# Kernel optimization log

Measured on AMD Instinct MI355X. Metric: run time of the kernel, lower is better.

The kernel has to match this reference:

```python
import jax, jax.numpy as jnp
import numpy as np

CHEB_K = 2  # chebyshev polynomial order (support_ks = [I, A] for cheb_k=2)


def _fc(x, w1, b1, w2, b2, w3, b3):
    # FC module: Linear -> sigmoid -> Linear -> sigmoid -> Linear
    h = jax.nn.sigmoid(x @ w1 + b1)
    h = jax.nn.sigmoid(h @ w2 + b2)
    return h @ w3 + b3


def _preprocess(adj):
    # adj: [B,N,N]; add self-loops then row-normalize
    adj = adj + jnp.eye(adj.shape[-1], dtype=adj.dtype)
    return adj / adj.sum(-1, keepdims=True)


def _gcn(x, adjs, ne, wpool, bpool):
    # x: [B,N,C], adjs: list of [B,N,N], ne: [N,E]
    # wpool: [E, 2*CHEB_K, C, O], bpool: [E, O]
    mats = []
    for A in adjs:
        ks = [jnp.broadcast_to(jnp.eye(A.shape[-1], dtype=A.dtype), A.shape), A]
        for _ in range(2, CHEB_K):
            ks.append(2.0 * jnp.matmul(A, ks[-1]) - ks[-2])
        mats.extend(ks)
    # [B,N,K,C] with K = 2*CHEB_K
    x_g = jnp.stack([jnp.einsum('bnm,bmc->bnc', S, x) for S in mats], axis=2)
    weights = jnp.einsum('nd,dkio->nkio', ne, wpool)  # [N,K,C,O]
    bias = ne @ bpool  # [N,O]
    return jnp.einsum('bnki,nkio->bno', x_g, weights) + bias


def _forward(x, state, ne0, ne1, ne2, fc1_w1, fc1_b1, fc1_w2, fc1_b2, fc1_w3, fc1_b3,
             fc2_w1, fc2_b1, fc2_w2, fc2_b2, fc2_w3, fc2_b3, gate_w, gate_b, upd_w, upd_b):
    hid = upd_w.shape[-1]
    ins = jnp.concatenate([x, state], axis=-1)  # [B,N,dim_in+hid]
    f1 = _fc(ins, fc1_w1, fc1_b1, fc1_w2, fc1_b2, fc1_w3, fc1_b3)  # [B,N,TD]
    f2 = _fc(ins, fc2_w1, fc2_b1, fc2_w2, fc2_b2, fc2_w3, fc2_b3)
    nv1 = jnp.tanh(ne0[:, None, :] * f1)  # einsum 'bd,bnd->bnd' == broadcast mul
    nv2 = jnp.tanh(ne1[:, None, :] * f2)
    adj = jnp.einsum('bnd,bmd->bnm', nv1, nv2) - jnp.einsum('bnd,bmd->bnm', nv2, nv1)
    adj1 = _preprocess(jax.nn.relu(adj))
    adj2 = _preprocess(jax.nn.relu(-jnp.swapaxes(adj, -2, -1)))
    z_r = jax.nn.sigmoid(_gcn(ins, [adj1, adj2], ne2, gate_w, gate_b))
    z, r = z_r[..., :hid], z_r[..., hid:]
    cand = jnp.concatenate([x, z * state], axis=-1)
    hc = jnp.tanh(_gcn(cand, [adj1, adj2], ne2, upd_w, upd_b))
    return r * state + (1.0 - r) * hc


def setup_inputs():
    B, N, DIN, DOUT, ED, TD = 32, 1024, 2, 64, 10, 32
    HG, MID = 16, 2  # hyperGNN_dim, middle_dim hardcoded in FC
    CIN = DIN + DOUT
    K2 = 2 * CHEB_K
    ks = jax.random.split(jax.random.key(0), 16)
    rn = lambda i, shape, s=1.0: jax.random.normal(ks[i], shape, dtype=jnp.float32) * s
    return {
        'x': rn(0, (B, N, DIN)),
        'state': rn(1, (B, N, DOUT)),
        'ne0': rn(2, (B, TD)),
        'ne1': rn(3, (B, TD)),
        'ne2': rn(4, (N, ED), 0.1),
        'fc1_w1': rn(5, (CIN, HG), 0.1), 'fc1_b1': jnp.zeros((HG,), jnp.float32),
        'fc1_w2': rn(6, (HG, MID), 0.1), 'fc1_b2': jnp.zeros((MID,), jnp.float32),
        'fc1_w3': rn(7, (MID, TD), 0.1), 'fc1_b3': jnp.zeros((TD,), jnp.float32),
        'fc2_w1': rn(8, (CIN, HG), 0.1), 'fc2_b1': jnp.zeros((HG,), jnp.float32),
        'fc2_w2': rn(9, (HG, MID), 0.1), 'fc2_b2': jnp.zeros((MID,), jnp.float32),
        'fc2_w3': rn(10, (MID, TD), 0.1), 'fc2_b3': jnp.zeros((TD,), jnp.float32),
        'gate_w': rn(11, (ED, K2, CIN, 2 * DOUT), 0.1),
        'gate_b': rn(12, (ED, 2 * DOUT), 0.1),
        'upd_w': rn(13, (ED, K2, CIN, DOUT), 0.1),
        'upd_b': rn(14, (ED, DOUT), 0.1),
    }


def reference(x, state, ne0, ne1, ne2, fc1_w1, fc1_b1, fc1_w2, fc1_b2, fc1_w3, fc1_b3,
              fc2_w1, fc2_b1, fc2_w2, fc2_b2, fc2_w3, fc2_b3, gate_w, gate_b, upd_w, upd_b):
    return _forward(x, state, ne0, ne1, ne2, fc1_w1, fc1_b1, fc1_w2, fc1_b2, fc1_w3, fc1_b3,
                    fc2_w1, fc2_b1, fc2_w2, fc2_b2, fc2_w3, fc2_b3, gate_w, gate_b, upd_w, upd_b)
```

## Files before the change

### kernel.cpp

```cpp
#include <hip/hip_runtime.h>
#include <math.h>

#define BB   32
#define NN   1024
#define DIN  2
#define DOUT 64
#define CIN  66
#define TD   32
#define ED   10
#define OG   128
#define OU   64
#define KP   160
#define XTR  80

typedef __bf16 bf16x8 __attribute__((ext_vector_type(8)));
typedef float  f32x4  __attribute__((ext_vector_type(4)));
typedef short  s16x8  __attribute__((ext_vector_type(8)));

__device__ __forceinline__ unsigned short f2b(float f) {
    __bf16 h = (__bf16)f;
    return *(unsigned short*)&h;
}

__device__ __forceinline__ unsigned int cvt_pk_bf16(float lo, float hi) {
    unsigned int r;
    asm("v_cvt_pk_bf16_f32 %0, %1, %2" : "=v"(r) : "v"(lo), "v"(hi));
    return r;
}
__device__ __forceinline__ void perm32swap(unsigned int& a, unsigned int& b) {
    asm("v_permlane32_swap_b32 %0, %1" : "+v"(a), "+v"(b));
}
__device__ __forceinline__ void perm16swap(unsigned int& a, unsigned int& b) {
    asm("v_permlane16_swap_b32 %0, %1" : "+v"(a), "+v"(b));
}

__global__ __launch_bounds__(256) void k_pre(
    const float* __restrict__ x, const float* __restrict__ state,
    const float* __restrict__ ne0, const float* __restrict__ ne1,
    const float* __restrict__ ne2,
    const float* __restrict__ w11, const float* __restrict__ b11,
    const float* __restrict__ w12, const float* __restrict__ b12,
    const float* __restrict__ w13, const float* __restrict__ b13,
    const float* __restrict__ w21, const float* __restrict__ b21,
    const float* __restrict__ w22, const float* __restrict__ b22,
    const float* __restrict__ w23, const float* __restrict__ b23,
    const float* __restrict__ gate_w, const float* __restrict__ gate_b,
    const float* __restrict__ upd_w, const float* __restrict__ upd_b,
    unsigned short* __restrict__ nv1b, unsigned short* __restrict__ nv2b,
    unsigned short* __restrict__ XT0, unsigned short* __restrict__ XT1,
    unsigned short* __restrict__ BcTg, unsigned short* __restrict__ BcTu,
    float* __restrict__ biasG, float* __restrict__ biasU)
{
    __shared__ float sw[2408];
    __shared__ unsigned short st[68*72];
    int blk = blockIdx.x;
    int t = threadIdx.x;

    if (blk < 128) {
        const int oW1 = 0, oB1 = 1056, oW2 = 1072, oB2 = 1104, oW3 = 1108, oB3 = 1172, F2 = 1204;
        for (int i = t; i < 1056; i += 256) { sw[oW1+i] = w11[i]; sw[F2+oW1+i] = w21[i]; }
        if (t < 16) { sw[oB1+t] = b11[t]; sw[F2+oB1+t] = b21[t]; }
        if (t < 32) { sw[oW2+t] = w12[t]; sw[F2+oW2+t] = w22[t]; }
        if (t < 2)  { sw[oB2+t] = b12[t]; sw[F2+oB2+t] = b22[t]; }
        if (t < 64) { sw[oW3+t] = w13[t]; sw[F2+oW3+t] = w23[t]; }
        if (t >= 64 && t < 96) { sw[oB3+t-64] = b13[t-64]; sw[F2+oB3+t-64] = b23[t-64]; }
        __syncthreads();

        int p = blk*256 + t;
        int b = p >> 10;

        float h1a[16], h1b[16];
        #pragma unroll
        for (int j = 0; j < 16; ++j) { h1a[j] = sw[oB1+j]; h1b[j] = sw[F2+oB1+j]; }
        for (int i = 0; i < CIN; ++i) {
            float v = (i < DIN) ? x[(size_t)p*DIN + i] : state[(size_t)p*DOUT + (i-DIN)];
            #pragma unroll
            for (int jq = 0; jq < 4; ++jq) {
                float4 wa = *(const float4*)&sw[oW1 + i*16 + jq*4];
                float4 wb = *(const float4*)&sw[F2 + oW1 + i*16 + jq*4];
                h1a[jq*4+0] += v*wa.x; h1a[jq*4+1] += v*wa.y;
                h1a[jq*4+2] += v*wa.z; h1a[jq*4+3] += v*wa.w;
                h1b[jq*4+0] += v*wb.x; h1b[jq*4+1] += v*wb.y;
                h1b[jq*4+2] += v*wb.z; h1b[jq*4+3] += v*wb.w;
            }
        }
        #pragma unroll
        for (int j = 0; j < 16; ++j) {
            h1a[j] = 1.f/(1.f + __expf(-h1a[j]));
            h1b[j] = 1.f/(1.f + __expf(-h1b[j]));
        }
        float h2a0 = sw[oB2+0], h2a1 = sw[oB2+1];
        float h2b0 = sw[F2+oB2+0], h2b1 = sw[F2+oB2+1];
        #pragma unroll
        for (int i = 0; i < 16; ++i) {
            h2a0 += h1a[i]*sw[oW2 + i*2 + 0];
            h2a1 += h1a[i]*sw[oW2 + i*2 + 1];
            h2b0 += h1b[i]*sw[F2+oW2 + i*2 + 0];
            h2b1 += h1b[i]*sw[F2+oW2 + i*2 + 1];
        }
        h2a0 = 1.f/(1.f + __expf(-h2a0)); h2a1 = 1.f/(1.f + __expf(-h2a1));
        h2b0 = 1.f/(1.f + __expf(-h2b0)); h2b1 = 1.f/(1.f + __expf(-h2b1));

        const float* pn0 = ne0 + b*TD;
        const float* pn1 = ne1 + b*TD;
        #pragma unroll
        for (int jq = 0; jq < 8; ++jq) {
            float4 ba  = *(const float4*)&sw[oB3 + jq*4];
            float4 wa0 = *(const float4*)&sw[oW3 + jq*4];
            float4 wa1 = *(const float4*)&sw[oW3 + 32 + jq*4];
            float4 bb2 = *(const float4*)&sw[F2+oB3 + jq*4];
            float4 wb0 = *(const float4*)&sw[F2+oW3 + jq*4];
            float4 wb1 = *(const float4*)&sw[F2+oW3 + 32 + jq*4];
            float4 n0 = *(const float4*)&pn0[jq*4];
            float4 n1 = *(const float4*)&pn1[jq*4];
            ushort4 u1, u2;
            u1.x = f2b(tanhf(n0.x*(ba.x + h2a0*wa0.x + h2a1*wa1.x)));
            u1.y = f2b(tanhf(n0.y*(ba.y + h2a0*wa0.y + h2a1*wa1.y)));
            u1.z = f2b(tanhf(n0.z*(ba.z + h2a0*wa0.z + h2a1*wa1.z)));
            u1.w = f2b(tanhf(n0.w*(ba.w + h2a0*wa0.w + h2a1*wa1.w)));
            u2.x = f2b(tanhf(n1.x*(bb2.x + h2b0*wb0.x + h2b1*wb1.x)));
            u2.y = f2b(tanhf(n1.y*(bb2.y + h2b0*wb0.y + h2b1*wb1.y)));
            u2.z = f2b(tanhf(n1.z*(bb2.z + h2b0*wb0.z + h2b1*wb1.z)));
            u2.w = f2b(tanhf(n1.w*(bb2.w + h2b0*wb0.w + h2b1*wb1.w)));
            *(ushort4*)&nv1b[(size_t)p*TD + jq*4] = u1;
            *(ushort4*)&nv2b[(size_t)p*TD + jq*4] = u2;
        }
    } else if (blk < 640) {
        int idx = blk - 128;
        int b = idx >> 4, m0 = (idx & 15)*64;
        for (int i = t; i < 1024; i += 256) {
            int m = i >> 4, cq = i & 15;
            size_t base = (size_t)b*NN + m0 + m;
            float4 v = *(const float4*)&state[base*DOUT + cq*4];
            st[(2 + cq*4 + 0)*72 + m] = f2b(v.x);
            st[(2 + cq*4 + 1)*72 + m] = f2b(v.y);
            st[(2 + cq*4 + 2)*72 + m] = f2b(v.z);
            st[(2 + cq*4 + 3)*72 + m] = f2b(v.w);
        }
        if (t < 128) {
            int m = t >> 1, c = t & 1;
            st[c*72 + m] = f2b(x[((size_t)b*NN + m0 + m)*DIN + c]);
        }
        __syncthreads();
        const unsigned int ONE2 = 0x3F803F80u;
        for (int i = t; i < XTR*8; i += 256) {
            int c = i >> 3, ch = i & 7;
            uint4 v;
            if (c < 66)      v = *(const uint4*)&st[c*72 + ch*8];
            else if (c == 66) v = make_uint4(ONE2, ONE2, ONE2, ONE2);
            else              v = make_uint4(0, 0, 0, 0);
            *(uint4*)&XT0[((size_t)b*XTR + c)*NN + m0 + ch*8] = v;
            if (c < 2 || c >= 66)
                *(uint4*)&XT1[((size_t)b*XTR + c)*NN + m0 + ch*8] = v;
        }
    } else if (blk < 1840) {
        int tid = (blk - 640)*256 + t;
        int c = tid / KP, k = tid - c*KP;
        const float* pool; int O, cc; unsigned short* dst;
        if (c < 1280) { pool = gate_w; O = OG; cc = c;        dst = BcTg; }
        else          { pool = upd_w;  O = OU; cc = c - 1280; dst = BcTu; }
        int d = cc / O, o = cc - d*O;
        float v = 0.f;
        if (k < 132) {
            int kp = (k < 66) ? 0 : 1;
            int i  = (k < 66) ? k : k - 66;
            v = pool[(size_t)((d*4 + kp)*CIN + i)*O + o]
              + pool[(size_t)((d*4 + kp + 2)*CIN + i)*O + o];
        }
        dst[(size_t)cc*KP + k] = f2b(v);
    } else {
        int i = (blk - 1840)*256 + t;
        int n = i / 192, j = i - n*192;
        float v = 0.f;
        if (j < 128) {
            #pragma unroll
            for (int d = 0; d < ED; ++d) v += ne2[(size_t)n*ED + d]*gate_b[d*OG + j];
            biasG[(size_t)n*OG + j] = v;
        } else {
            int o = j - 128;
            #pragma unroll
            for (int d = 0; d < ED; ++d) v += ne2[(size_t)n*ED + d]*upd_b[d*OU + o];
            biasU[(size_t)n*OU + o] = v;
        }
    }
}

__global__ __launch_bounds__(256) void k_aapply(
    const unsigned short* __restrict__ nv1b, const unsigned short* __restrict__ nv2b,
    const unsigned short* __restrict__ XTg, unsigned short* __restrict__ A)
{
    __shared__ unsigned short s_nv1c[2][2560];
    __shared__ unsigned short s_nv2c[2][2560];
    __shared__ unsigned short s_xt[2][5760];

    int t = threadIdx.x;
    int id = blockIdx.x;
    int b = id & 31, rbase = (id >> 5)*64;
    int w = t >> 6, lane = t & 63, lq = lane >> 4, ln = lane & 15;

    bf16x8 a1 = *(const bf16x8*)&nv1b[((size_t)b*NN + rbase + 16*w + ln)*TD + lq*8];
    s16x8 a2s = *(const s16x8*)&nv2b[((size_t)b*NN + rbase + 16*w + ln)*TD + lq*8];
    const s16x8 sgn = {(short)0x8000,(short)0x8000,(short)0x8000,(short)0x8000,
                       (short)0x8000,(short)0x8000,(short)0x8000,(short)0x8000};
    a2s ^= sgn;
    bf16x8 a2n = (bf16x8)a2s;

    const unsigned short* pnv1 = nv1b + (size_t)b*NN*TD;
    const unsigned short* pnv2 = nv2b + (size_t)b*NN*TD;
    const unsigned short* pxt  = XTg  + (size_t)b*XTR*NN;
    int nnode = t >> 2;
    int nch   = (t & 3)*8;
    int xc    = t >> 3;
    int xch   = (t & 7)*8;

    uint4 q0, q1, r0, r1, r2;

    f32x4 acc[5];
    #pragma unroll
    for (int k = 0; k < 5; ++k) acc[k] = (f32x4){0.f,0.f,0.f,0.f};
    const f32x4 zero4 = {0.f,0.f,0.f,0.f};
    union U8 { unsigned int u[4]; bf16x8 v; };

    q0 = *(const uint4*)&pnv1[(size_t)nnode*TD + nch];
    q1 = *(const uint4*)&pnv2[(size_t)nnode*TD + nch];
    r0 = *(const uint4*)&pxt[(size_t)xc*NN + xch];
    r1 = *(const uint4*)&pxt[(size_t)(xc+32)*NN + xch];
    if (t < 128) r2 = *(const uint4*)&pxt[(size_t)(xc+64)*NN + xch];
    *(uint4*)&s_nv1c[0][nnode*40 + nch] = q0;
    *(uint4*)&s_nv2c[0][nnode*40 + nch] = q1;
    *(uint4*)&s_xt[0][xc*72 + xch] = r0;
    *(uint4*)&s_xt[0][(xc+32)*72 + xch] = r1;
    if (t < 128) *(uint4*)&s_xt[0][(xc+64)*72 + xch] = r2;
    q0 = *(const uint4*)&pnv1[(size_t)(64 + nnode)*TD + nch];
    q1 = *(const uint4*)&pnv2[(size_t)(64 + nnode)*TD + nch];
    r0 = *(const uint4*)&pxt[(size_t)xc*NN + 64 + xch];
    r1 = *(const uint4*)&pxt[(size_t)(xc+32)*NN + 64 + xch];
    if (t < 128) r2 = *(const uint4*)&pxt[(size_t)(xc+64)*NN + 64 + xch];
    __syncthreads();

    int cur = 0;
    for (int mb = 0; mb < NN; mb += 64) {
        if (mb + 64 < NN) {
            *(uint4*)&s_nv1c[cur^1][nnode*40 + nch] = q0;
            *(uint4*)&s_nv2c[cur^1][nnode*40 + nch] = q1;
            *(uint4*)&s_xt[cur^1][xc*72 + xch] = r0;
            *(uint4*)&s_xt[cur^1][(xc+32)*72 + xch] = r1;
            if (t < 128) *(uint4*)&s_xt[cur^1][(xc+64)*72 + xch] = r2;
        }
        if (mb + 128 < NN) {
            int mb2 = mb + 128;
            q0 = *(const uint4*)&pnv1[(size_t)(mb2 + nnode)*TD + nch];
            q1 = *(const uint4*)&pnv2[(size_t)(mb2 + nnode)*TD + nch];
            r0 = *(const uint4*)&pxt[(size_t)xc*NN + mb2 + xch];
            r1 = *(const uint4*)&pxt[(size_t)(xc+32)*NN + mb2 + xch];
            if (t < 128) r2 = *(const uint4*)&pxt[(size_t)(xc+64)*NN + mb2 + xch];
        }

        unsigned int u[4][2];
        #pragma unroll
        for (int jj = 0; jj < 4; ++jj) {
            bf16x8 b2 = *(const bf16x8*)&s_nv2c[cur][(jj*16 + ln)*40 + lq*8];
            bf16x8 b1 = *(const bf16x8*)&s_nv1c[cur][(jj*16 + ln)*40 + lq*8];
            f32x4 s = __builtin_amdgcn_mfma_f32_16x16x32_bf16(b2, a1,  zero4, 0, 0, 0);
            s       = __builtin_amdgcn_mfma_f32_16x16x32_bf16(b1, a2n, s,     0, 0, 0);
            u[jj][0] = cvt_pk_bf16(fmaxf(s[0], 0.f), fmaxf(s[1], 0.f));
            u[jj][1] = cvt_pk_bf16(fmaxf(s[2], 0.f), fmaxf(s[3], 0.f));
        }

        unsigned int w00 = u[0][0], w20 = u[1][0]; perm32swap(w00, w20); perm16swap(w00, w20);
        unsigned int w01 = u[0][1], w21 = u[1][1]; perm32swap(w01, w21); perm16swap(w01, w21);
        unsigned int x00 = u[2][0], x20 = u[3][0]; perm32swap(x00, x20); perm16swap(x00, x20);
        unsigned int x01 = u[2][1], x21 = u[3][1]; perm32swap(x01, x21); perm16swap(x01, x21);
        U8 p0, p1;
        p0.u[0] = w00; p0.u[1] = w01; p0.u[2] = w20; p0.u[3] = w21;
        p1.u[0] = x00; p1.u[1] = x01; p1.u[2] = x20; p1.u[3] = x21;
        bf16x8 pa0 = p0.v, pa1 = p1.v;

        #pragma unroll
        for (int k = 0; k < 5; ++k) {
            bf16x8 xb0 = *(const bf16x8*)&s_xt[cur][(k*16 + ln)*72 +      lq*8];
            bf16x8 xb1 = *(const bf16x8*)&s_xt[cur][(k*16 + ln)*72 + 32 + lq*8];
            acc[k] = __builtin_amdgcn_mfma_f32_16x16x32_bf16(pa0, xb0, acc[k], 0, 0, 0);
            acc[k] = __builtin_amdgcn_mfma_f32_16x16x32_bf16(pa1, xb1, acc[k], 0, 0, 0);
        }

        __syncthreads();
        cur ^= 1;
    }

    float rinv[4];
    #pragma unroll
    for (int r = 0; r < 4; ++r) {
        float rs = __shfl(acc[4][r], (lane & 48) | 2, 64);
        rinv[r] = 1.0f / (1.0f + rs);
    }

    #pragma unroll
    for (int k = 0; k < 5; ++k) {
        int c = k*16 + ln;
        if (c < CIN) {
            #pragma unroll
            for (int r = 0; r < 4; ++r) {
                int gr = rbase + 16*w + lq*4 + r;
                size_t rowG = (size_t)b*NN + gr;
                unsigned short xu = XTg[((size_t)b*XTR + c)*NN + gr];
                float xr = (float)(*(const __bf16*)&xu);
                A[rowG*KP + c]      = xu;
                A[rowG*KP + 66 + c] = f2b((acc[k][r] + xr) * rinv[r]);
            }
        }
    }
    for (int i = t; i < 64*28; i += 256) {
        int rr = i / 28, cc = 132 + (i - 28*(i/28));
        A[((size_t)b*NN + rbase + rr)*KP + cc] = 0;
    }
}

template<int O, int MODE>
__global__ __launch_bounds__(256) void k_gemm(
    const unsigned short* __restrict__ A, const unsigned short* __restrict__ BcT,
    const float* __restrict__ ne2, const float* __restrict__ biasP,
    const float* __restrict__ state, unsigned short* __restrict__ XT1,
    float* __restrict__ rbuf, float* __restrict__ out)
{
    __shared__ unsigned short s_b[80*168];

    int t = threadIdx.x;
    int w = t >> 6, lane = t & 63, lq = lane >> 4, ln = lane & 15;
    int o0 = blockIdx.y*16;
    int rowBlock = blockIdx.x*128;
    int rowW = rowBlock + w*32;

    f32x4 acc[2][2][5];
    #pragma unroll
    for (int h = 0; h < 2; ++h)
        #pragma unroll
        for (int f = 0; f < 2; ++f)
            #pragma unroll
            for (int c = 0; c < 5; ++c) acc[h][f][c] = (f32x4){0.f,0.f,0.f,0.f};

    #pragma unroll
    for (int h = 0; h < 2; ++h) {
        if (h) __syncthreads();
        for (int i = t; i < 1600; i += 256) {
            int cc = i / 20, kc = i - cc*20;
            int d = h*5 + (cc >> 4), oo = cc & 15;
            *(uint4*)&s_b[cc*168 + kc*8] =
                *(const uint4*)&BcT[(size_t)(d*O + o0 + oo)*KP + kc*8];
        }
        __syncthreads();

        #pragma unroll
        for (int kc = 0; kc < 5; ++kc) {
            bf16x8 af0 = *(const bf16x8*)&A[(size_t)(rowW      + ln)*KP + kc*32 + lq*8];
            bf16x8 af1 = *(const bf16x8*)&A[(size_t)(rowW + 16 + ln)*KP + kc*32 + lq*8];
            #pragma unroll
            for (int ct = 0; ct < 5; ++ct) {
                bf16x8 bf = *(const bf16x8*)&s_b[(ct*16 + ln)*168 + kc*32 + lq*8];
                acc[h][0][ct] = __builtin_amdgcn_mfma_f32_16x16x32_bf16(af0, bf, acc[h][0][ct], 0, 0, 0);
                acc[h][1][ct] = __builtin_amdgcn_mfma_f32_16x16x32_bf16(af1, bf, acc[h][1][ct], 0, 0, 0);
            }
        }
    }

    int o = o0 + ln;
    #pragma unroll
    for (int f = 0; f < 2; ++f) {
        #pragma unroll
        for (int r = 0; r < 4; ++r) {
            int row_l = w*32 + 16*f + lq*4 + r;
            size_t rowG = (size_t)rowBlock + row_l;
            int n = (int)(rowG & (NN - 1));
            int bb = (int)(rowG >> 10);
            const float* nep = &ne2[(size_t)n*ED];
            float val = biasP[(size_t)n*O + o];
            #pragma unroll
            for (int d = 0; d < 5; ++d) val += nep[d]     * acc[0][f][d][r];
            #pragma unroll
            for (int d = 0; d < 5; ++d) val += nep[5 + d] * acc[1][f][d][r];
            if (MODE == 0) {
                float sv = 1.f/(1.f + __expf(-val));
                if (o0 < 64) {
                    float zst = sv * state[rowG*DOUT + o];
                    XT1[((size_t)bb*XTR + 2 + o)*NN + n] = f2b(zst);
                } else {
                    rbuf[rowG*DOUT + (o - 64)] = sv;
                }
            } else {
                float hc = tanhf(val);
                float rg = rbuf[rowG*DOUT + o];
                float st = state[rowG*DOUT + o];
                out[rowG*DOUT + o] = rg*st + (1.f - rg)*hc;
            }
        }
    }
}

extern "C" void kernel_launch(void* const* d_in, const int* in_sizes, int n_in,
                              void* d_out, int out_size, void* d_ws, size_t ws_size,
                              hipStream_t stream)
{
    const float* x      = (const float*)d_in[0];
    const float* state  = (const float*)d_in[1];
    const float* ne0    = (const float*)d_in[2];
    const float* ne1    = (const float*)d_in[3];
    const float* ne2    = (const float*)d_in[4];
    const float* f1w1   = (const float*)d_in[5];
    const float* f1b1   = (const float*)d_in[6];
    const float* f1w2   = (const float*)d_in[7];
    const float* f1b2   = (const float*)d_in[8];
    const float* f1w3   = (const float*)d_in[9];
    const float* f1b3   = (const float*)d_in[10];
    const float* f2w1   = (const float*)d_in[11];
    const float* f2b1   = (const float*)d_in[12];
    const float* f2w2   = (const float*)d_in[13];
    const float* f2b2   = (const float*)d_in[14];
    const float* f2w3   = (const float*)d_in[15];
    const float* f2b3   = (const float*)d_in[16];
    const float* gate_w = (const float*)d_in[17];
    const float* gate_b = (const float*)d_in[18];
    const float* upd_w  = (const float*)d_in[19];
    const float* upd_b  = (const float*)d_in[20];

    unsigned short* nv1b = (unsigned short*)d_ws;
    unsigned short* nv2b = nv1b + (size_t)BB*NN*TD;
    unsigned short* XT0  = nv2b + (size_t)BB*NN*TD;
    unsigned short* XT1  = XT0  + (size_t)BB*XTR*NN;
    unsigned short* A    = XT1  + (size_t)BB*XTR*NN;
    unsigned short* BcTg = A    + (size_t)BB*NN*KP;
    unsigned short* BcTu = BcTg + (size_t)1280*KP;
    float* biasG = (float*)(BcTu + (size_t)640*KP);
    float* biasU = biasG + (size_t)NN*OG;
    float* rbuf  = biasU + (size_t)NN*OU;
    float* out   = (float*)d_out;

    k_pre<<<dim3(2608), 256, 0, stream>>>(x, state, ne0, ne1, ne2,
        f1w1, f1b1, f1w2, f1b2, f1w3, f1b3,
        f2w1, f2b1, f2w2, f2b2, f2w3, f2b3,
        gate_w, gate_b, upd_w, upd_b,
        nv1b, nv2b, XT0, XT1, BcTg, BcTu, biasG, biasU);

    k_aapply<<<dim3(512), 256, 0, stream>>>(nv1b, nv2b, XT0, A);

    k_gemm<OG,0><<<dim3(BB*NN/128, 8), 256, 0, stream>>>(A, BcTg, ne2, biasG,
                                                         state, XT1, rbuf, nullptr);

    k_aapply<<<dim3(512), 256, 0, stream>>>(nv1b, nv2b, XT1, A);

    k_gemm<OU,1><<<dim3(BB*NN/128, 4), 256, 0, stream>>>(A, BcTu, ne2, biasU,
                                                         state, nullptr, rbuf, out);
}
```

Measured before the change: 222.0 us.

## Stage A tile in LDS once and loop over output tiles with double-buffered B

The GEMM kernel previously launched one block per (row tile, 16-column output tile) and re-read the A rows from global memory for every output tile. Now each block loads its 128-row A tile into shared memory once and iterates over all output tiles. It prefetches the next B slice into registers while computing on the current one, with double-buffered LDS for B. This cuts redundant A traffic but shrinks the grid to 256 blocks, raises LDS use, and serializes output tiles per block, which may reduce occupancy and parallelism.

```diff
diff --git a/kernel.cpp b/kernel.cpp
--- a/kernel.cpp
+++ b/kernel.cpp
@@ -316,6 +316,50 @@
     }
 }
 
+__device__ __forceinline__ void gemm_half(
+    const unsigned short* sa, const unsigned short* sbh,
+    f32x4 (&acc)[2][5], int w, int lq, int ln)
+{
+    #pragma unroll
+    for (int kc = 0; kc < 5; ++kc) {
+        bf16x8 af0 = *(const bf16x8*)&sa[(w*32      + ln)*168 + kc*32 + lq*8];
+        bf16x8 af1 = *(const bf16x8*)&sa[(w*32 + 16 + ln)*168 + kc*32 + lq*8];
+        #pragma unroll
+        for (int ct = 0; ct < 5; ++ct) {
+            bf16x8 bf = *(const bf16x8*)&sbh[(ct*16 + ln)*168 + kc*32 + lq*8];
+            acc[0][ct] = __builtin_amdgcn_mfma_f32_16x16x32_bf16(af0, bf, acc[0][ct], 0, 0, 0);
+            acc[1][ct] = __builtin_amdgcn_mfma_f32_16x16x32_bf16(af1, bf, acc[1][ct], 0, 0, 0);
+        }
+    }
+}
+
+__device__ __forceinline__ void loadB(
+    const unsigned short* __restrict__ BcT, int O, int o0, int h, int t,
+    uint4 (&pr)[7])
+{
+    #pragma unroll
+    for (int k = 0; k < 7; ++k) {
+        int i = k*256 + t;
+        if (i < 1600) {
+            int cc = i/20, kc = i - cc*20;
+            int d = h*5 + (cc >> 4), oo = cc & 15;
+            pr[k] = *(const uint4*)&BcT[(size_t)(d*O + o0 + oo)*KP + kc*8];
+        }
+    }
+}
+
+__device__ __forceinline__ void writeB(unsigned short* sb, int t, const uint4 (&pr)[7])
+{
+    #pragma unroll
+    for (int k = 0; k < 7; ++k) {
+        int i = k*256 + t;
+        if (i < 1600) {
+            int cc = i/20, kc = i - cc*20;
+            *(uint4*)&sb[cc*168 + kc*8] = pr[k];
+        }
+    }
+}
+
 template<int O, int MODE>
 __global__ __launch_bounds__(256) void k_gemm(
     const unsigned short* __restrict__ A, const unsigned short* __restrict__ BcT,
@@ -323,76 +367,78 @@
     const float* __restrict__ state, unsigned short* __restrict__ XT1,
     float* __restrict__ rbuf, float* __restrict__ out)
 {
-    __shared__ unsigned short s_b[80*168];
-
+    __shared__ unsigned short s_a[128*168];
+    __shared__ unsigned short s_b[2][80*168];
+
+    const int NT = O/16;
     int t = threadIdx.x;
     int w = t >> 6, lane = t & 63, lq = lane >> 4, ln = lane & 15;
-    int o0 = blockIdx.y*16;
     int rowBlock = blockIdx.x*128;
-    int rowW = rowBlock + w*32;
-
-    f32x4 acc[2][2][5];
-    #pragma unroll
-    for (int h = 0; h < 2; ++h)
+
+    for (int i = t; i < 2560; i += 256) {
+        int r = i/20, kc = i - r*20;
+        *(uint4*)&s_a[r*168 + kc*8] = *(const uint4*)&A[(size_t)(rowBlock + r)*KP + kc*8];
+    }
+    for (int i = t; i < 1600; i += 256) {
+        int cc = i/20, kc = i - cc*20;
+        int d = (cc >> 4), oo = cc & 15;
+        *(uint4*)&s_b[0][cc*168 + kc*8] = *(const uint4*)&BcT[(size_t)(d*O + oo)*KP + kc*8];
+    }
+    uint4 pr[7];
+    loadB(BcT, O, 0, 1, t, pr);
+    __syncthreads();
+
+    for (int ot = 0; ot < NT; ++ot) {
+        f32x4 accA[2][5], accB[2][5];
         #pragma unroll
         for (int f = 0; f < 2; ++f)
             #pragma unroll
-            for (int c = 0; c < 5; ++c) acc[h][f][c] = (f32x4){0.f,0.f,0.f,0.f};
-
-    #pragma unroll
-    for (int h = 0; h < 2; ++h) {
-        if (h) __syncthreads();
-        for (int i = t; i < 1600; i += 256) {
-            int cc = i / 20, kc = i - cc*20;
-            int d = h*5 + (cc >> 4), oo = cc & 15;
-            *(uint4*)&s_b[cc*168 + kc*8] =
-                *(const uint4*)&BcT[(size_t)(d*O + o0 + oo)*KP + kc*8];
-        }
+            for (int c = 0; c < 5; ++c) {
+                accA[f][c] = (f32x4){0.f,0.f,0.f,0.f};
+                accB[f][c] = (f32x4){0.f,0.f,0.f,0.f};
+            }
+
+        writeB(&s_b[1][0], t, pr);
+        if (ot + 1 < NT) loadB(BcT, O, (ot+1)*16, 0, t, pr);
+        gemm_half(s_a, &s_b[0][0], accA, w, lq, ln);
         __syncthreads();
 
-        #pragma unroll
-        for (int kc = 0; kc < 5; ++kc) {
-            bf16x8 af0 = *(const bf16x8*)&A[(size_t)(rowW      + ln)*KP + kc*32 + lq*8];
-            bf16x8 af1 = *(const bf16x8*)&A[(size_t)(rowW + 16 + ln)*KP + kc*32 + lq*8];
-            #pragma unroll
-            for (int ct = 0; ct < 5; ++ct) {
-                bf16x8 bf = *(const bf16x8*)&s_b[(ct*16 + ln)*168 + kc*32 + lq*8];
-                acc[h][0][ct] = __builtin_amdgcn_mfma_f32_16x16x32_bf16(af0, bf, acc[h][0][ct], 0, 0, 0);
-                acc[h][1][ct] = __builtin_amdgcn_mfma_f32_16x16x32_bf16(af1, bf, acc[h][1][ct], 0, 0, 0);
+        if (ot + 1 < NT) writeB(&s_b[0][0], t, pr);
+        if (ot + 1 < NT) loadB(BcT, O, (ot+1)*16, 1, t, pr);
+        gemm_half(s_a, &s_b[1][0], accB, w, lq, ln);
+
+        int o = ot*16 + ln;
+        #pragma unroll
+        for (int f = 0; f < 2; ++f) {
+            #pragma unroll
+            for (int r = 0; r < 4; ++r) {
+                int row_l = w*32 + 16*f + lq*4 + r;
+                size_t rowG = (size_t)rowBlock + row_l;
+                int n = (int)(rowG & (NN - 1));
+                int bb = (int)(rowG >> 10);
+                const float* nep = &ne2[(size_t)n*ED];
+                float val = biasP[(size_t)n*O + o];
+                #pragma unroll
+                for (int d = 0; d < 5; ++d) val += nep[d]     * accA[f][d][r];
+                #pragma unroll
+                for (int d = 0; d < 5; ++d) val += nep[5 + d] * accB[f][d][r];
+                if (MODE == 0) {
+                    float sv = 1.f/(1.f + __expf(-val));
+                    if (o < 64) {
+                        float zst = sv * state[rowG*DOUT + o];
+                        XT1[((size_t)bb*XTR + 2 + o)*NN + n] = f2b(zst);
+                    } else {
+                        rbuf[rowG*DOUT + (o - 64)] = sv;
+                    }
+                } else {
+                    float hc = tanhf(val);
+                    float rg = rbuf[rowG*DOUT + o];
+                    float st = state[rowG*DOUT + o];
+                    out[rowG*DOUT + o] = rg*st + (1.f - rg)*hc;
+                }
             }
         }
-    }
-
-    int o = o0 + ln;
-    #pragma unroll
-    for (int f = 0; f < 2; ++f) {
-        #pragma unroll
-        for (int r = 0; r < 4; ++r) {
-            int row_l = w*32 + 16*f + lq*4 + r;
-            size_t rowG = (size_t)rowBlock + row_l;
-            int n = (int)(rowG & (NN - 1));
-            int bb = (int)(rowG >> 10);
-            const float* nep = &ne2[(size_t)n*ED];
-            float val = biasP[(size_t)n*O + o];
-            #pragma unroll
-            for (int d = 0; d < 5; ++d) val += nep[d]     * acc[0][f][d][r];
-            #pragma unroll
-            for (int d = 0; d < 5; ++d) val += nep[5 + d] * acc[1][f][d][r];
-            if (MODE == 0) {
-                float sv = 1.f/(1.f + __expf(-val));
-                if (o0 < 64) {
-                    float zst = sv * state[rowG*DOUT + o];
-                    XT1[((size_t)bb*XTR + 2 + o)*NN + n] = f2b(zst);
-                } else {
-                    rbuf[rowG*DOUT + (o - 64)] = sv;
-                }
-            } else {
-                float hc = tanhf(val);
-                float rg = rbuf[rowG*DOUT + o];
-                float st = state[rowG*DOUT + o];
-                out[rowG*DOUT + o] = rg*st + (1.f - rg)*hc;
-            }
-        }
+        __syncthreads();
     }
 }
 
@@ -442,11 +488,11 @@
 
     k_aapply<<<dim3(512), 256, 0, stream>>>(nv1b, nv2b, XT0, A);
 
-    k_gemm<OG,0><<<dim3(BB*NN/128, 8), 256, 0, stream>>>(A, BcTg, ne2, biasG,
-                                                         state, XT1, rbuf, nullptr);
+    k_gemm<OG,0><<<dim3(256), 256, 0, stream>>>(A, BcTg, ne2, biasG,
+                                                state, XT1, rbuf, nullptr);
 
     k_aapply<<<dim3(512), 256, 0, stream>>>(nv1b, nv2b, XT1, A);
 
-    k_gemm<OU,1><<<dim3(BB*NN/128, 4), 256, 0, stream>>>(A, BcTu, ne2, biasU,
-                                                         state, nullptr, rbuf, out);
-}
+    k_gemm<OU,1><<<dim3(256), 256, 0, stream>>>(A, BcTu, ne2, biasU,
+                                                state, nullptr, rbuf, out);
+}
```

Result: slower. 300.5 us (+35.4%).
